# Optimization experiments

Measured on AMD Instinct MI355X. Metric: run time of the kernel, lower is better.

Reference implementation:

```python
import jax, jax.numpy as jnp
import numpy as np

NUM_EXPERTS = 8
TOP_K = 2
IN_DIM = 2048
BOT_DIM = 512
BATCH, SEQ = 4, 2048


def setup_inputs() -> dict:
    key = jax.random.key(0)
    ks = jax.random.split(key, 8)
    scale_d = 1.0 / np.sqrt(IN_DIM)
    scale_b = 1.0 / np.sqrt(BOT_DIM)
    return {
        "hidden_states": jax.random.normal(ks[0], (BATCH, SEQ, IN_DIM), jnp.float32),
        # gate: nn.Linear(in_dim, num_experts, bias=False) -> weight [E, D]
        "gate_w": jax.random.normal(ks[1], (NUM_EXPERTS, IN_DIM), jnp.float32) * scale_d,
        # routed experts: down weight [E, B, D], down bias [E, B], up weight [E, D, B], up bias [E, D]
        # (original inits up weights/biases to zero; use small random so grads are non-trivial)
        "wd": jax.random.normal(ks[2], (NUM_EXPERTS, BOT_DIM, IN_DIM), jnp.float32) * scale_d,
        "bd": jnp.zeros((NUM_EXPERTS, BOT_DIM), jnp.float32),
        "wu": jax.random.normal(ks[3], (NUM_EXPERTS, IN_DIM, BOT_DIM), jnp.float32) * scale_b * 0.02,
        "bu": jnp.zeros((NUM_EXPERTS, IN_DIM), jnp.float32),
        # one shared Bottleneck_adapter
        "ws_d": jax.random.normal(ks[4], (BOT_DIM, IN_DIM), jnp.float32) * scale_d,
        "bs_d": jnp.zeros((BOT_DIM,), jnp.float32),
        "ws_u": jax.random.normal(ks[5], (IN_DIM, BOT_DIM), jnp.float32) * scale_b * 0.02,
        "bs_u": jnp.zeros((IN_DIM,), jnp.float32),
    }


def _gelu(x):
    # torch.nn.GELU() default = exact erf form
    return jax.nn.gelu(x, approximate=False)


def reference(hidden_states, gate_w, wd, bd, wu, bu, ws_d, bs_d, ws_u, bs_u):
    B, S, D = hidden_states.shape
    x = hidden_states.reshape(-1, D)                      # [T, D]
    T = x.shape[0]

    # --- top-k softmax routing (softmax in fp32, renormalize top-k weights) ---
    logits = x @ gate_w.T                                 # [T, E]
    probs = jax.nn.softmax(logits.astype(jnp.float32), axis=-1)
    rw, sel = jax.lax.top_k(probs, TOP_K)                 # [T, K]
    rw = rw / rw.sum(axis=-1, keepdims=True)
    rw = rw.astype(x.dtype)

    # dense combine weights [T, E]: zero for unselected experts == skipping them
    combine = jnp.zeros((T, NUM_EXPERTS), x.dtype).at[
        jnp.arange(T)[:, None], sel
    ].add(rw)

    # --- routed experts: bottleneck FFN per expert, combined by routing weight ---
    down = jnp.einsum('td,ebd->teb', x, wd) + bd[None]    # [T, E, Bn]
    h = _gelu(down) * combine[:, :, None]                 # weight before up-proj (linear)
    expert_out = jnp.einsum('teb,edb->td', h, wu) + combine @ bu  # [T, D]

    # --- shared expert (applied to original hidden states) ---
    shared = _gelu(x @ ws_d.T + bs_d) @ ws_u.T + bs_u

    out = (expert_out + shared).reshape(B, S, D)
    return out
```

## Files before the change

kernel.cpp:

```cpp
#include <hip/hip_runtime.h>
#include <hip/hip_bf16.h>

typedef __bf16 bf16_t;
typedef __bf16 bf16x8 __attribute__((ext_vector_type(8)));
typedef float f32x4 __attribute__((ext_vector_type(4)));

#define T_TOK 8192
#define D_IN  2048
#define D_BOT 512
#define MAXTILES 192
#define MAXDTILES 200

union U4B8 { uint4 u; bf16x8 b; };
__device__ __forceinline__ bf16x8 as_bf16x8(uint4 u) { U4B8 x; x.u = u; return x.b; }
__device__ __forceinline__ uint4 as_uint4(bf16x8 b) { U4B8 x; x.b = b; return x.u; }

typedef const __attribute__((address_space(1))) void gas_void;
typedef __attribute__((address_space(3))) void las_void;
__device__ __forceinline__ void async16(const void* g, void* l) {
    __builtin_amdgcn_global_load_lds((gas_void*)g, (las_void*)l, 16, 0, 0);
}

__device__ __forceinline__ uint4 ld_cvt8(const float* __restrict__ p) {
    f32x4 a0 = ((const f32x4*)p)[0];
    f32x4 a1 = ((const f32x4*)p)[1];
    bf16x8 v;
    v[0] = (bf16_t)a0[0]; v[1] = (bf16_t)a0[1]; v[2] = (bf16_t)a0[2]; v[3] = (bf16_t)a0[3];
    v[4] = (bf16_t)a1[0]; v[5] = (bf16_t)a1[1]; v[6] = (bf16_t)a1[2]; v[7] = (bf16_t)a1[3];
    return as_uint4(v);
}

__device__ __forceinline__ float gelu_f(float v) {
    return 0.5f * v * (1.0f + erff(v * 0.7071067811865476f));
}

__global__ __launch_bounds__(256) void cvt_kernel(const float* __restrict__ src,
                                                  bf16_t* __restrict__ dst, int n8) {
    const int i = blockIdx.x * 256 + threadIdx.x;
    if (i < n8) ((uint4*)dst)[i] = ld_cvt8(src + (size_t)i * 8);
}

__global__ __launch_bounds__(256) void gate_kernel(const float* __restrict__ x,
                                                   const float* __restrict__ gw,
                                                   float* __restrict__ combine,
                                                   int* __restrict__ sel,
                                                   bf16_t* __restrict__ Xbf) {
    const int wave = threadIdx.x >> 6, lane = threadIdx.x & 63;
    const int t = blockIdx.x * 4 + wave;
    const float* xrow = x + (size_t)t * D_IN;
    f32x4 xa[4][2];
#pragma unroll
    for (int c = 0; c < 4; ++c) {
        const float* p = xrow + c * 512 + lane * 8;
        xa[c][0] = ((const f32x4*)p)[0];
        xa[c][1] = ((const f32x4*)p)[1];
    }
#pragma unroll
    for (int c = 0; c < 4; ++c) {
        bf16x8 v;
#pragma unroll
        for (int j = 0; j < 4; ++j) { v[j] = (bf16_t)xa[c][0][j]; v[4 + j] = (bf16_t)xa[c][1][j]; }
        *(uint4*)(Xbf + (size_t)t * D_IN + c * 512 + lane * 8) = as_uint4(v);
    }
    float p[8];
#pragma unroll
    for (int e = 0; e < 8; ++e) {
        const float* gr = gw + e * D_IN;
        float s = 0.f;
#pragma unroll
        for (int c = 0; c < 4; ++c) {
            const float* q = gr + c * 512 + lane * 8;
            f32x4 g0 = ((const f32x4*)q)[0], g1 = ((const f32x4*)q)[1];
#pragma unroll
            for (int j = 0; j < 4; ++j) s += xa[c][0][j] * g0[j] + xa[c][1][j] * g1[j];
        }
#pragma unroll
        for (int off = 32; off > 0; off >>= 1) s += __shfl_xor(s, off, 64);
        p[e] = s;
    }
    float m = p[0];
#pragma unroll
    for (int e = 1; e < 8; ++e) m = fmaxf(m, p[e]);
    float sum = 0.f;
#pragma unroll
    for (int e = 0; e < 8; ++e) { p[e] = expf(p[e] - m); sum += p[e]; }
    const float inv = 1.0f / sum;
#pragma unroll
    for (int e = 0; e < 8; ++e) p[e] *= inv;
    int i0 = 0;
#pragma unroll
    for (int e = 1; e < 8; ++e) if (p[e] > p[i0]) i0 = e;
    int i1 = -1;
#pragma unroll
    for (int e = 0; e < 8; ++e) { if (e == i0) continue; if (i1 < 0 || p[e] > p[i1]) i1 = e; }
    const float rs = 1.0f / (p[i0] + p[i1]);
    if (lane < 8)
        combine[t * 8 + lane] = (lane == i0) ? p[i0] * rs : (lane == i1) ? p[i1] * rs : 0.0f;
    if (lane == 0) sel[t] = i0 | (i1 << 4);
}

__global__ __launch_bounds__(256) void build_kernel(const int* __restrict__ sel,
                                                    int* __restrict__ meta,
                                                    int* __restrict__ tokE,
                                                    int* __restrict__ tokP) {
    __shared__ unsigned short cAll[8][256];
    __shared__ unsigned short cP[64][256];
    const int tid = threadIdx.x;
#pragma unroll
    for (int e = 0; e < 8; ++e) cAll[e][tid] = 0;
#pragma unroll
    for (int p = 0; p < 64; ++p) cP[p][tid] = 0;
    __syncthreads();
    int sl[32];
#pragma unroll
    for (int j = 0; j < 32; ++j) sl[j] = sel[tid * 32 + j];
#pragma unroll
    for (int j = 0; j < 32; ++j) {
        const int e0 = sl[j] & 15, e1 = sl[j] >> 4;
        cAll[e0][tid]++; cAll[e1][tid]++; cP[e0 * 8 + e1][tid]++;
    }
    __syncthreads();
    if (tid < 8) {
        unsigned short* arr = cAll[tid];
        int run = 0;
        for (int i = 0; i < 256; ++i) { int v = arr[i]; arr[i] = (unsigned short)run; run += v; }
        meta[tid] = run;
    } else if (tid >= 64 && tid < 128) {
        unsigned short* arr = cP[tid - 64];
        int run = 0;
        for (int i = 0; i < 256; ++i) { int v = arr[i]; arr[i] = (unsigned short)run; run += v; }
        meta[64 + (tid - 64)] = run;
    }
    __syncthreads();
    if (tid == 0) {
        int nt = 0;
        for (int p = 0; p < 64; ++p) {
            const int c = meta[64 + p];
            for (int s = 0; s < c; s += 64) { meta[128 + nt] = p; meta[320 + nt] = s; ++nt; }
        }
        meta[8] = nt;
        int nd = 0;
        for (int e = 0; e < 9; ++e) {
            const int c = (e < 8) ? meta[e] : T_TOK;
            for (int s = 0; s < c; s += 128) { meta[512 + nd] = e; meta[768 + nd] = s; ++nd; }
        }
        meta[9] = nd;
    }
#pragma unroll
    for (int j = 0; j < 32; ++j) {
        const int t = tid * 32 + j, e0 = sl[j] & 15, e1 = sl[j] >> 4;
        const int p0 = cAll[e0][tid]++;  tokE[e0 * 8192 + p0] = t;
        const int p1 = cAll[e1][tid]++;  tokE[e1 * 8192 + p1] = t | 65536;
        const int q  = cP[e0 * 8 + e1][tid]++;  tokP[(e0 * 8 + e1) * 8192 + q] = t;
    }
}

__global__ __launch_bounds__(256) void down_kernel(const bf16_t* __restrict__ Xbf,
                                                   const bf16_t* __restrict__ Wall,
                                                   const float* __restrict__ Bd,
                                                   const float* __restrict__ Bsd,
                                                   const float* __restrict__ combine,
                                                   const int* __restrict__ meta,
                                                   const int* __restrict__ tokE,
                                                   bf16_t* __restrict__ Ht) {
    __shared__ uint4 As4[128 * 8];
    __shared__ uint4 Bs4[64 * 8];
    const int yt = blockIdx.x;
    if (yt >= meta[9]) return;
    const int e = meta[512 + yt];
    const int m0 = meta[768 + yt];
    const int count = (e < 8) ? meta[e] : T_TOK;
    const int tid = threadIdx.x, lane = tid & 63, wv = tid >> 6;
    const int wm = wv >> 1, wn = wv & 1;
    const int tile_n = blockIdx.y * 64;
    const int gB = (lane & 7) ^ ((lane >> 3) & 7);

    const bf16_t* aAddr[4];
    const bf16_t* bAddr[2];
#pragma unroll
    for (int j = 0; j < 4; ++j) {
        const int rr = (wv * 4 + j) * 8 + (lane >> 3);
        int gi = m0 + rr; if (gi > count - 1) gi = count - 1;
        const int t = (e < 8) ? (tokE[e * 8192 + gi] & 0xFFFF) : gi;
        aAddr[j] = Xbf + (size_t)t * D_IN + gB * 8;
    }
#pragma unroll
    for (int j = 0; j < 2; ++j) {
        const int rr = (wv * 2 + j) * 8 + (lane >> 3);
        bAddr[j] = Wall + (size_t)(e * 512 + tile_n + rr) * D_IN + gB * 8;
    }

    f32x4 acc[4][2];
#pragma unroll
    for (int i = 0; i < 4; ++i)
#pragma unroll
        for (int j = 0; j < 2; ++j) acc[i][j] = (f32x4){0.f, 0.f, 0.f, 0.f};

    for (int kt = 0; kt < D_IN / 64; ++kt) {
        const int k0 = kt * 64;
#pragma unroll
        for (int j = 0; j < 4; ++j)
            async16(aAddr[j] + k0, &As4[(wv * 4 + j) * 64]);
#pragma unroll
        for (int j = 0; j < 2; ++j)
            async16(bAddr[j] + k0, &Bs4[(wv * 2 + j) * 64]);
        __syncthreads();
#pragma unroll
        for (int ks = 0; ks < 2; ++ks) {
            bf16x8 af[4], bfr[2];
#pragma unroll
            for (int i = 0; i < 4; ++i) {
                const int ar = wm * 64 + i * 16 + (lane & 15);
                af[i] = as_bf16x8(As4[ar * 8 + ((ks * 4 + (lane >> 4)) ^ (lane & 7))]);
            }
#pragma unroll
            for (int i = 0; i < 2; ++i) {
                const int br = wn * 32 + i * 16 + (lane & 15);
                bfr[i] = as_bf16x8(Bs4[br * 8 + ((ks * 4 + (lane >> 4)) ^ (lane & 7))]);
            }
#pragma unroll
            for (int mi = 0; mi < 4; ++mi)
#pragma unroll
                for (int nj = 0; nj < 2; ++nj)
                    acc[mi][nj] = __builtin_amdgcn_mfma_f32_16x16x32_bf16(
                        af[mi], bfr[nj], acc[mi][nj], 0, 0, 0);
        }
        __syncthreads();
    }

#pragma unroll
    for (int nj = 0; nj < 2; ++nj) {
        const int nn = tile_n + wn * 32 + nj * 16 + (lane & 15);
        const float bias = (e < 8) ? Bd[e * 512 + nn] : Bsd[nn];
#pragma unroll
        for (int mi = 0; mi < 4; ++mi) {
            const int g0 = m0 + wm * 64 + mi * 16 + ((lane >> 4) << 2);
#pragma unroll
            for (int r = 0; r < 4; ++r) {
                const int gi = g0 + r;
                if (gi >= count) continue;
                if (e < 8) {
                    const int entry = tokE[e * 8192 + gi];
                    const int t = entry & 0xFFFF, rank = entry >> 16;
                    const float v = gelu_f(acc[mi][nj][r] + bias) * combine[t * 8 + e];
                    Ht[(size_t)t * 1536 + rank * 512 + nn] = (bf16_t)v;
                } else {
                    Ht[(size_t)gi * 1536 + 1024 + nn] = (bf16_t)gelu_f(acc[mi][nj][r] + bias);
                }
            }
        }
    }
}

__global__ __launch_bounds__(256) void up_kernel(const bf16_t* __restrict__ Ht,
                                                 const bf16_t* __restrict__ Wup,
                                                 const float* __restrict__ Bu,
                                                 const float* __restrict__ Bsu,
                                                 const float* __restrict__ combine,
                                                 const int* __restrict__ meta,
                                                 const int* __restrict__ tokP,
                                                 float* __restrict__ Out) {
    __shared__ uint4 As4[64 * 8];
    __shared__ uint4 Bs4[128 * 8];
    const int yt = blockIdx.x;
    if (yt >= meta[8]) return;
    const int p = meta[128 + yt], s = meta[320 + yt];
    const int e0 = p >> 3, e1 = p & 7;
    const int cntP = meta[64 + p];
    const int tid = threadIdx.x, lane = tid & 63, wv = tid >> 6;
    const int wm = wv >> 1, wn = wv & 1;
    const int tile_n = blockIdx.y * 128;
    const int gB = (lane & 7) ^ ((lane >> 3) & 7);

    const bf16_t* aAddr[2];
#pragma unroll
    for (int j = 0; j < 2; ++j) {
        const int rr = (wv * 2 + j) * 8 + (lane >> 3);
        int gi = s + rr; if (gi > cntP - 1) gi = cntP - 1;
        const int t = tokP[p * 8192 + gi];
        aAddr[j] = Ht + (size_t)t * 1536 + gB * 8;
    }
    size_t bRow[4];
#pragma unroll
    for (int j = 0; j < 4; ++j) {
        const int rr = (wv * 4 + j) * 8 + (lane >> 3);
        bRow[j] = (size_t)(tile_n + rr) * D_BOT + gB * 8;
    }

    f32x4 acc[2][4];
#pragma unroll
    for (int i = 0; i < 2; ++i)
#pragma unroll
        for (int j = 0; j < 4; ++j) acc[i][j] = (f32x4){0.f, 0.f, 0.f, 0.f};

    for (int kt = 0; kt < 24; ++kt) {
        const int seg = kt >> 3;
        const int slot = (seg == 0) ? e0 : (seg == 1) ? e1 : 8;
        const bf16_t* wbase = Wup + (size_t)slot * (D_IN * D_BOT) + (kt & 7) * 64;
#pragma unroll
        for (int j = 0; j < 2; ++j)
            async16(aAddr[j] + kt * 64, &As4[(wv * 2 + j) * 64]);
#pragma unroll
        for (int j = 0; j < 4; ++j)
            async16(wbase + bRow[j], &Bs4[(wv * 4 + j) * 64]);
        __syncthreads();
#pragma unroll
        for (int ks = 0; ks < 2; ++ks) {
            bf16x8 af[2], bfr[4];
#pragma unroll
            for (int i = 0; i < 2; ++i) {
                const int ar = wm * 32 + i * 16 + (lane & 15);
                af[i] = as_bf16x8(As4[ar * 8 + ((ks * 4 + (lane >> 4)) ^ (lane & 7))]);
            }
#pragma unroll
            for (int i = 0; i < 4; ++i) {
                const int br = wn * 64 + i * 16 + (lane & 15);
                bfr[i] = as_bf16x8(Bs4[br * 8 + ((ks * 4 + (lane >> 4)) ^ (lane & 7))]);
            }
#pragma unroll
            for (int mi = 0; mi < 2; ++mi)
#pragma unroll
                for (int nj = 0; nj < 4; ++nj)
                    acc[mi][nj] = __builtin_amdgcn_mfma_f32_16x16x32_bf16(
                        af[mi], bfr[nj], acc[mi][nj], 0, 0, 0);
        }
        __syncthreads();
    }

#pragma unroll
    for (int nj = 0; nj < 4; ++nj) {
        const int d = tile_n + wn * 64 + nj * 16 + (lane & 15);
        const float bu0 = Bu[e0 * D_IN + d], bu1 = Bu[e1 * D_IN + d], bs = Bsu[d];
#pragma unroll
        for (int mi = 0; mi < 2; ++mi) {
            const int r0 = wm * 32 + mi * 16 + ((lane >> 4) << 2);
#pragma unroll
            for (int r = 0; r < 4; ++r) {
                const int gi = s + r0 + r;
                if (gi >= cntP) continue;
                const int t = tokP[p * 8192 + gi];
                const float c0 = combine[t * 8 + e0], c1 = combine[t * 8 + e1];
                Out[(size_t)t * D_IN + d] = acc[mi][nj][r] + c0 * bu0 + c1 * bu1 + bs;
            }
        }
    }
}

extern "C" void kernel_launch(void* const* d_in, const int* in_sizes, int n_in,
                              void* d_out, int out_size, void* d_ws, size_t ws_size,
                              hipStream_t stream) {
    const float* x   = (const float*)d_in[0];
    const float* gw  = (const float*)d_in[1];
    const float* wd  = (const float*)d_in[2];
    const float* bd  = (const float*)d_in[3];
    const float* wu  = (const float*)d_in[4];
    const float* bu  = (const float*)d_in[5];
    const float* wsd = (const float*)d_in[6];
    const float* bsd = (const float*)d_in[7];
    const float* wsu = (const float*)d_in[8];
    const float* bsu = (const float*)d_in[9];
    float* out = (float*)d_out;

    char* ws = (char*)d_ws;
    float* combine = (float*)(ws + 0);
    int*   meta    = (int*)(ws + 262144);
    int*   sel     = (int*)(ws + 266240);
    int*   tokE    = (int*)(ws + 299008);
    int*   tokP    = (int*)(ws + 561152);
    bf16_t* Xbf    = (bf16_t*)(ws + 2658304);
    bf16_t* Ht     = (bf16_t*)(ws + 36212736ull);
    bf16_t* Wall   = (bf16_t*)(ws + 61378560ull);

    gate_kernel<<<T_TOK / 4, 256, 0, stream>>>(x, gw, combine, sel, Xbf);
    build_kernel<<<1, 256, 0, stream>>>(sel, meta, tokE, tokP);

    cvt_kernel<<<(4096 * D_IN / 8) / 256, 256, 0, stream>>>(wd, Wall, 4096 * D_IN / 8);
    cvt_kernel<<<(512 * D_IN / 8) / 256, 256, 0, stream>>>(wsd, Wall + (size_t)4096 * D_IN, 512 * D_IN / 8);

    down_kernel<<<dim3(MAXDTILES, 8), 256, 0, stream>>>(Xbf, Wall, bd, bsd, combine, meta, tokE, Ht);

    cvt_kernel<<<(8 * D_IN * D_BOT / 8) / 256, 256, 0, stream>>>(wu, Wall, 8 * D_IN * D_BOT / 8);
    cvt_kernel<<<(D_IN * D_BOT / 8) / 256, 256, 0, stream>>>(wsu, Wall + (size_t)8 * D_IN * D_BOT, D_IN * D_BOT / 8);

    up_kernel<<<dim3(MAXTILES, 16), 256, 0, stream>>>(Ht, Wall, bu, bsu, combine, meta, tokP, out);
}
```

Baseline: 482.2 us.

## Widen up-projection N tile to 256 and fuse weight conversions into one launch

The up-projection kernel now computes a 256-wide output tile per block instead of 128, doubling B-tile shared memory and per-wave accumulators. This halves the grid in y and the number of times each gathered Ht row is reloaded. When the workspace is large enough, the four fp32-to-bf16 weight conversions are merged into a single launch writing to separate down and up buffers, which removes launch overhead and the dependency that forced the up conversion to wait for the down kernel. The wider tile raises register pressure and may lower occupancy.

New measurement: 506.6 us. 1.05x slower.

```diff
diff --git a/kernel.cpp b/kernel.cpp
--- a/kernel.cpp
+++ b/kernel.cpp
@@ -38,6 +38,23 @@
                                                   bf16_t* __restrict__ dst, int n8) {
     const int i = blockIdx.x * 256 + threadIdx.x;
     if (i < n8) ((uint4*)dst)[i] = ld_cvt8(src + (size_t)i * 8);
+}
+
+__global__ __launch_bounds__(256) void cvt4_kernel(const float* __restrict__ wd,
+                                                   const float* __restrict__ wsd,
+                                                   const float* __restrict__ wu,
+                                                   const float* __restrict__ wsu,
+                                                   bf16_t* __restrict__ WallD,
+                                                   bf16_t* __restrict__ WallU) {
+    const int i = blockIdx.x * 256 + threadIdx.x;
+    const int N0 = 4096 * 2048 / 8;
+    const int N1 = N0 + 512 * 2048 / 8;
+    const int N2 = N1 + 8 * 2048 * 512 / 8;
+    const int N3 = N2 + 2048 * 512 / 8;
+    if (i < N0)      ((uint4*)WallD)[i] = ld_cvt8(wd + (size_t)i * 8);
+    else if (i < N1) ((uint4*)WallD)[i] = ld_cvt8(wsd + (size_t)(i - N0) * 8);
+    else if (i < N2) ((uint4*)WallU)[i - N1] = ld_cvt8(wu + (size_t)(i - N1) * 8);
+    else if (i < N3) ((uint4*)WallU)[i - N1] = ld_cvt8(wsu + (size_t)(i - N2) * 8);
 }
 
 __global__ __launch_bounds__(256) void gate_kernel(const float* __restrict__ x,
@@ -261,7 +278,7 @@
                                                  const int* __restrict__ tokP,
                                                  float* __restrict__ Out) {
     __shared__ uint4 As4[64 * 8];
-    __shared__ uint4 Bs4[128 * 8];
+    __shared__ uint4 Bs4[256 * 8];
     const int yt = blockIdx.x;
     if (yt >= meta[8]) return;
     const int p = meta[128 + yt], s = meta[320 + yt];
@@ -269,7 +286,7 @@
     const int cntP = meta[64 + p];
     const int tid = threadIdx.x, lane = tid & 63, wv = tid >> 6;
     const int wm = wv >> 1, wn = wv & 1;
-    const int tile_n = blockIdx.y * 128;
+    const int tile_n = blockIdx.y * 256;
     const int gB = (lane & 7) ^ ((lane >> 3) & 7);
 
     const bf16_t* aAddr[2];
@@ -280,47 +297,45 @@
         const int t = tokP[p * 8192 + gi];
         aAddr[j] = Ht + (size_t)t * 1536 + gB * 8;
     }
-    size_t bRow[4];
-#pragma unroll
-    for (int j = 0; j < 4; ++j) {
-        const int rr = (wv * 4 + j) * 8 + (lane >> 3);
-        bRow[j] = (size_t)(tile_n + rr) * D_BOT + gB * 8;
-    }
-
-    f32x4 acc[2][4];
+    int brr[8];
+#pragma unroll
+    for (int j = 0; j < 8; ++j)
+        brr[j] = tile_n + (wv * 8 + j) * 8 + (lane >> 3);
+
+    f32x4 acc[2][8];
 #pragma unroll
     for (int i = 0; i < 2; ++i)
 #pragma unroll
-        for (int j = 0; j < 4; ++j) acc[i][j] = (f32x4){0.f, 0.f, 0.f, 0.f};
+        for (int j = 0; j < 8; ++j) acc[i][j] = (f32x4){0.f, 0.f, 0.f, 0.f};
 
     for (int kt = 0; kt < 24; ++kt) {
         const int seg = kt >> 3;
         const int slot = (seg == 0) ? e0 : (seg == 1) ? e1 : 8;
-        const bf16_t* wbase = Wup + (size_t)slot * (D_IN * D_BOT) + (kt & 7) * 64;
+        const bf16_t* wbase = Wup + (size_t)slot * (D_IN * D_BOT) + (kt & 7) * 64 + gB * 8;
 #pragma unroll
         for (int j = 0; j < 2; ++j)
             async16(aAddr[j] + kt * 64, &As4[(wv * 2 + j) * 64]);
 #pragma unroll
-        for (int j = 0; j < 4; ++j)
-            async16(wbase + bRow[j], &Bs4[(wv * 4 + j) * 64]);
+        for (int j = 0; j < 8; ++j)
+            async16(wbase + (size_t)brr[j] * D_BOT, &Bs4[(wv * 8 + j) * 64]);
         __syncthreads();
 #pragma unroll
         for (int ks = 0; ks < 2; ++ks) {
-            bf16x8 af[2], bfr[4];
+            bf16x8 af[2], bfr[8];
 #pragma unroll
             for (int i = 0; i < 2; ++i) {
                 const int ar = wm * 32 + i * 16 + (lane & 15);
                 af[i] = as_bf16x8(As4[ar * 8 + ((ks * 4 + (lane >> 4)) ^ (lane & 7))]);
             }
 #pragma unroll
-            for (int i = 0; i < 4; ++i) {
-                const int br = wn * 64 + i * 16 + (lane & 15);
+            for (int i = 0; i < 8; ++i) {
+                const int br = wn * 128 + i * 16 + (lane & 15);
                 bfr[i] = as_bf16x8(Bs4[br * 8 + ((ks * 4 + (lane >> 4)) ^ (lane & 7))]);
             }
 #pragma unroll
             for (int mi = 0; mi < 2; ++mi)
 #pragma unroll
-                for (int nj = 0; nj < 4; ++nj)
+                for (int nj = 0; nj < 8; ++nj)
                     acc[mi][nj] = __builtin_amdgcn_mfma_f32_16x16x32_bf16(
                         af[mi], bfr[nj], acc[mi][nj], 0, 0, 0);
         }
@@ -328,8 +343,8 @@
     }
 
 #pragma unroll
-    for (int nj = 0; nj < 4; ++nj) {
-        const int d = tile_n + wn * 64 + nj * 16 + (lane & 15);
+    for (int nj = 0; nj < 8; ++nj) {
+        const int d = tile_n + wn * 128 + nj * 16 + (lane & 15);
         const float bu0 = Bu[e0 * D_IN + d], bu1 = Bu[e1 * D_IN + d], bs = Bsu[d];
 #pragma unroll
         for (int mi = 0; mi < 2; ++mi) {
@@ -369,18 +384,24 @@
     int*   tokP    = (int*)(ws + 561152);
     bf16_t* Xbf    = (bf16_t*)(ws + 2658304);
     bf16_t* Ht     = (bf16_t*)(ws + 36212736ull);
-    bf16_t* Wall   = (bf16_t*)(ws + 61378560ull);
+    bf16_t* WallD  = (bf16_t*)(ws + 61378560ull);
+    const size_t NEED_SEP = 61378560ull + 2ull * 18874368ull;
+    const bool separate = (ws_size >= NEED_SEP);
+    bf16_t* WallU  = separate ? (bf16_t*)(ws + 61378560ull + 18874368ull) : WallD;
 
     gate_kernel<<<T_TOK / 4, 256, 0, stream>>>(x, gw, combine, sel, Xbf);
     build_kernel<<<1, 256, 0, stream>>>(sel, meta, tokE, tokP);
 
-    cvt_kernel<<<(4096 * D_IN / 8) / 256, 256, 0, stream>>>(wd, Wall, 4096 * D_IN / 8);
-    cvt_kernel<<<(512 * D_IN / 8) / 256, 256, 0, stream>>>(wsd, Wall + (size_t)4096 * D_IN, 512 * D_IN / 8);
-
-    down_kernel<<<dim3(MAXDTILES, 8), 256, 0, stream>>>(Xbf, Wall, bd, bsd, combine, meta, tokE, Ht);
-
-    cvt_kernel<<<(8 * D_IN * D_BOT / 8) / 256, 256, 0, stream>>>(wu, Wall, 8 * D_IN * D_BOT / 8);
-    cvt_kernel<<<(D_IN * D_BOT / 8) / 256, 256, 0, stream>>>(wsu, Wall + (size_t)8 * D_IN * D_BOT, D_IN * D_BOT / 8);
-
-    up_kernel<<<dim3(MAXTILES, 16), 256, 0, stream>>>(Ht, Wall, bu, bsu, combine, meta, tokP, out);
-}
+    if (separate) {
+        cvt4_kernel<<<9216, 256, 0, stream>>>(wd, wsd, wu, wsu, WallD, WallU);
+        down_kernel<<<dim3(MAXDTILES, 8), 256, 0, stream>>>(Xbf, WallD, bd, bsd, combine, meta, tokE, Ht);
+        up_kernel<<<dim3(MAXTILES, 8), 256, 0, stream>>>(Ht, WallU, bu, bsu, combine, meta, tokP, out);
+    } else {
+        cvt_kernel<<<(4096 * D_IN / 8) / 256, 256, 0, stream>>>(wd, WallD, 4096 * D_IN / 8);
+        cvt_kernel<<<(512 * D_IN / 8) / 256, 256, 0, stream>>>(wsd, WallD + (size_t)4096 * D_IN, 512 * D_IN / 8);
+        down_kernel<<<dim3(MAXDTILES, 8), 256, 0, stream>>>(Xbf, WallD, bd, bsd, combine, meta, tokE, Ht);
+        cvt_kernel<<<(8 * D_IN * D_BOT / 8) / 256, 256, 0, stream>>>(wu, WallD, 8 * D_IN * D_BOT / 8);
+        cvt_kernel<<<(D_IN * D_BOT / 8) / 256, 256, 0, stream>>>(wsu, WallD + (size_t)8 * D_IN * D_BOT, D_IN * D_BOT / 8);
+        up_kernel<<<dim3(MAXTILES, 8), 256, 0, stream>>>(Ht, WallD, bu, bsu, combine, meta, tokP, out);
+    }
+}
```

## Swizzle GEMM block order for XCD locality and fuse weight conversions

Applied to the files above, without the earlier changes.

Down and up GEMM grids are flattened to 1D and remapped so that consecutive blocks on the same XCD (blockIdx mod 8) cover all N-tiles of the same token tile, improving L2 reuse of the gathered activation rows. When the workspace is large enough, all four weight fp32->bf16 conversions run in one launch into separate down/up buffers, removing three launches and the serialization between down GEMM and the up-weight conversion. This needs extra workspace and falls back to the old path otherwise.

Measured after the change: 450.9 us. -6.5%, faster.

```diff
diff --git a/kernel.cpp b/kernel.cpp
--- a/kernel.cpp
+++ b/kernel.cpp
@@ -38,6 +38,23 @@
                                                   bf16_t* __restrict__ dst, int n8) {
     const int i = blockIdx.x * 256 + threadIdx.x;
     if (i < n8) ((uint4*)dst)[i] = ld_cvt8(src + (size_t)i * 8);
+}
+
+__global__ __launch_bounds__(256) void cvt4_kernel(const float* __restrict__ wd,
+                                                   const float* __restrict__ wsd,
+                                                   const float* __restrict__ wu,
+                                                   const float* __restrict__ wsu,
+                                                   bf16_t* __restrict__ WallD,
+                                                   bf16_t* __restrict__ WallU) {
+    const int i = blockIdx.x * 256 + threadIdx.x;
+    const int N0 = 4096 * 2048 / 8;
+    const int N1 = N0 + 512 * 2048 / 8;
+    const int N2 = N1 + 8 * 2048 * 512 / 8;
+    const int N3 = N2 + 2048 * 512 / 8;
+    if (i < N0)      ((uint4*)WallD)[i] = ld_cvt8(wd + (size_t)i * 8);
+    else if (i < N1) ((uint4*)WallD)[i] = ld_cvt8(wsd + (size_t)(i - N0) * 8);
+    else if (i < N2) ((uint4*)WallU)[i - N1] = ld_cvt8(wu + (size_t)(i - N1) * 8);
+    else if (i < N3) ((uint4*)WallU)[i - N1] = ld_cvt8(wsu + (size_t)(i - N2) * 8);
 }
 
 __global__ __launch_bounds__(256) void gate_kernel(const float* __restrict__ x,
@@ -165,14 +182,16 @@
                                                    bf16_t* __restrict__ Ht) {
     __shared__ uint4 As4[128 * 8];
     __shared__ uint4 Bs4[64 * 8];
-    const int yt = blockIdx.x;
+    const int orig = blockIdx.x;
+    const int swz = (orig & 7) * 200 + (orig >> 3);
+    const int yt = swz >> 3;
+    const int tile_n = (swz & 7) * 64;
     if (yt >= meta[9]) return;
     const int e = meta[512 + yt];
     const int m0 = meta[768 + yt];
     const int count = (e < 8) ? meta[e] : T_TOK;
     const int tid = threadIdx.x, lane = tid & 63, wv = tid >> 6;
     const int wm = wv >> 1, wn = wv & 1;
-    const int tile_n = blockIdx.y * 64;
     const int gB = (lane & 7) ^ ((lane >> 3) & 7);
 
     const bf16_t* aAddr[4];
@@ -262,14 +281,16 @@
                                                  float* __restrict__ Out) {
     __shared__ uint4 As4[64 * 8];
     __shared__ uint4 Bs4[128 * 8];
-    const int yt = blockIdx.x;
+    const int orig = blockIdx.x;
+    const int swz = (orig & 7) * 384 + (orig >> 3);
+    const int yt = swz >> 4;
+    const int tile_n = (swz & 15) * 128;
     if (yt >= meta[8]) return;
     const int p = meta[128 + yt], s = meta[320 + yt];
     const int e0 = p >> 3, e1 = p & 7;
     const int cntP = meta[64 + p];
     const int tid = threadIdx.x, lane = tid & 63, wv = tid >> 6;
     const int wm = wv >> 1, wn = wv & 1;
-    const int tile_n = blockIdx.y * 128;
     const int gB = (lane & 7) ^ ((lane >> 3) & 7);
 
     const bf16_t* aAddr[2];
@@ -369,18 +390,24 @@
     int*   tokP    = (int*)(ws + 561152);
     bf16_t* Xbf    = (bf16_t*)(ws + 2658304);
     bf16_t* Ht     = (bf16_t*)(ws + 36212736ull);
-    bf16_t* Wall   = (bf16_t*)(ws + 61378560ull);
+    bf16_t* WallD  = (bf16_t*)(ws + 61378560ull);
+    const size_t NEED_SEP = 61378560ull + 2ull * 18874368ull;
+    const bool separate = (ws_size >= NEED_SEP);
+    bf16_t* WallU  = separate ? (bf16_t*)(ws + 61378560ull + 18874368ull) : WallD;
 
     gate_kernel<<<T_TOK / 4, 256, 0, stream>>>(x, gw, combine, sel, Xbf);
     build_kernel<<<1, 256, 0, stream>>>(sel, meta, tokE, tokP);
 
-    cvt_kernel<<<(4096 * D_IN / 8) / 256, 256, 0, stream>>>(wd, Wall, 4096 * D_IN / 8);
-    cvt_kernel<<<(512 * D_IN / 8) / 256, 256, 0, stream>>>(wsd, Wall + (size_t)4096 * D_IN, 512 * D_IN / 8);
-
-    down_kernel<<<dim3(MAXDTILES, 8), 256, 0, stream>>>(Xbf, Wall, bd, bsd, combine, meta, tokE, Ht);
-
-    cvt_kernel<<<(8 * D_IN * D_BOT / 8) / 256, 256, 0, stream>>>(wu, Wall, 8 * D_IN * D_BOT / 8);
-    cvt_kernel<<<(D_IN * D_BOT / 8) / 256, 256, 0, stream>>>(wsu, Wall + (size_t)8 * D_IN * D_BOT, D_IN * D_BOT / 8);
-
-    up_kernel<<<dim3(MAXTILES, 16), 256, 0, stream>>>(Ht, Wall, bu, bsu, combine, meta, tokP, out);
-}
+    if (separate) {
+        cvt4_kernel<<<9216, 256, 0, stream>>>(wd, wsd, wu, wsu, WallD, WallU);
+        down_kernel<<<MAXDTILES * 8, 256, 0, stream>>>(Xbf, WallD, bd, bsd, combine, meta, tokE, Ht);
+        up_kernel<<<MAXTILES * 16, 256, 0, stream>>>(Ht, WallU, bu, bsu, combine, meta, tokP, out);
+    } else {
+        cvt_kernel<<<(4096 * D_IN / 8) / 256, 256, 0, stream>>>(wd, WallD, 4096 * D_IN / 8);
+        cvt_kernel<<<(512 * D_IN / 8) / 256, 256, 0, stream>>>(wsd, WallD + (size_t)4096 * D_IN, 512 * D_IN / 8);
+        down_kernel<<<MAXDTILES * 8, 256, 0, stream>>>(Xbf, WallD, bd, bsd, combine, meta, tokE, Ht);
+        cvt_kernel<<<(8 * D_IN * D_BOT / 8) / 256, 256, 0, stream>>>(wu, WallD, 8 * D_IN * D_BOT / 8);
+        cvt_kernel<<<(D_IN * D_BOT / 8) / 256, 256, 0, stream>>>(wsu, WallD + (size_t)8 * D_IN * D_BOT, D_IN * D_BOT / 8);
+        up_kernel<<<MAXTILES * 16, 256, 0, stream>>>(Ht, WallD, bu, bsu, combine, meta, tokP, out);
+    }
+}
```
